# Kernel optimization log

Measured on AMD Instinct MI355X. Metric: run time of the kernel, lower is better.

## Reference

```python
import jax, jax.numpy as jnp
import numpy as np

NUM_CAPSULES = 10
NUM_ROUTES = 512
IN_CHANNELS = 8
OUT_CHANNELS = 16
BATCH = 512  # must equal NUM_ROUTES for the module's broadcast to be valid


def squash(x):
    # norm over last dim; v = ||s||^2/(1+||s||^2) * s/||s||
    norm = jnp.linalg.norm(x, axis=-1, keepdims=True)
    norm_sq = norm ** 2
    return norm_sq / (1.0 + norm_sq) * (x / norm)


def setup_inputs() -> dict:
    key = jax.random.key(0)
    k1, k2 = jax.random.split(key)
    x = jax.random.normal(k1, (BATCH, NUM_ROUTES, IN_CHANNELS), dtype=jnp.float32)
    route_weights = jax.random.normal(
        k2, (NUM_CAPSULES, NUM_ROUTES, IN_CHANNELS, OUT_CHANNELS), dtype=jnp.float32
    )
    return {"x": x, "route_weights": route_weights}


def reference(x, route_weights):
    B, R, Cin = x.shape
    # x -> [B, 1, R, Cin] (after view/unsqueeze/permute in the torch code)
    xb = x[:, None, :, :]
    # route_weights.permute(1,0,2,3) -> [R, num_caps, Cin, Cout]
    w = jnp.transpose(route_weights, (1, 0, 2, 3))
    # torch/jnp matmul broadcast of batch dims (B,1) vs (R,num_caps); B==R here.
    # u_hat[b, j] = x[b] @ w[route=b, cap=j]  -> [B, num_caps, R, Cout]
    u_hat = jnp.matmul(xb, w)
    b_ij = jnp.zeros(u_hat.shape[:3] + (1,), dtype=u_hat.dtype)
    for _ in range(3):  # fixed 3 routing iterations
        c_ij = jax.nn.softmax(b_ij, axis=2)            # softmax over routes
        s_j = jnp.sum(c_ij * u_hat, axis=2, keepdims=True)  # [B,J,1,Cout]
        v_j = squash(s_j)
        b_ij = b_ij + jnp.sum(u_hat * v_j, axis=-1, keepdims=True)
    return jnp.squeeze(v_j, axis=2)  # [B, num_caps, Cout]
```

## Files before the change

### kernel.cpp

```cpp
#include <hip/hip_runtime.h>
#include <math.h>

constexpr int BATCH = 512;
constexpr int NC    = 10;
constexpr int RR    = 512;
constexpr int CI    = 8;
constexpr int CO    = 16;

constexpr int TPB = 128;
constexpr int RPT = RR / TPB;

__global__ __launch_bounds__(TPB) void caps_route_kernel(
    const float* __restrict__ x,
    const float* __restrict__ rw,
    float* __restrict__ out)
{
    const int blk  = blockIdx.x;
    const int b    = blk / NC;
    const int c    = blk - b * NC;
    const int t    = threadIdx.x;
    const int lane = t & 63;
    const int wave = t >> 6;

    __shared__ __align__(16) float W[CI][CO];
    __shared__ __align__(16) float red[2][CO];
    __shared__ float sred[2];

    if (t < CI * CO) {
        ((float*)W)[t] = rw[((size_t)c * RR + b) * (CI * CO) + t];
    }
    __syncthreads();

    float xs[RPT][CI];
    #pragma unroll
    for (int k = 0; k < RPT; ++k) {
        const float4* xp = (const float4*)(x + ((size_t)b * RR + t + k * TPB) * CI);
        float4 a0 = xp[0], a1 = xp[1];
        xs[k][0]=a0.x; xs[k][1]=a0.y; xs[k][2]=a0.z; xs[k][3]=a0.w;
        xs[k][4]=a1.x; xs[k][5]=a1.y; xs[k][6]=a1.z; xs[k][7]=a1.w;
    }

    float u[RPT][CO];
    #pragma unroll
    for (int k = 0; k < RPT; ++k)
        #pragma unroll
        for (int o = 0; o < CO; ++o) u[k][o] = 0.f;

    #pragma unroll
    for (int i = 0; i < CI; ++i) {
        const float4* Wrow = (const float4*)&W[i][0];
        float4 wa = Wrow[0], wb = Wrow[1], wc = Wrow[2], wd = Wrow[3];
        #pragma unroll
        for (int k = 0; k < RPT; ++k) {
            const float xv = xs[k][i];
            u[k][0]  = fmaf(xv, wa.x, u[k][0]);
            u[k][1]  = fmaf(xv, wa.y, u[k][1]);
            u[k][2]  = fmaf(xv, wa.z, u[k][2]);
            u[k][3]  = fmaf(xv, wa.w, u[k][3]);
            u[k][4]  = fmaf(xv, wb.x, u[k][4]);
            u[k][5]  = fmaf(xv, wb.y, u[k][5]);
            u[k][6]  = fmaf(xv, wb.z, u[k][6]);
            u[k][7]  = fmaf(xv, wb.w, u[k][7]);
            u[k][8]  = fmaf(xv, wc.x, u[k][8]);
            u[k][9]  = fmaf(xv, wc.y, u[k][9]);
            u[k][10] = fmaf(xv, wc.z, u[k][10]);
            u[k][11] = fmaf(xv, wc.w, u[k][11]);
            u[k][12] = fmaf(xv, wd.x, u[k][12]);
            u[k][13] = fmaf(xv, wd.y, u[k][13]);
            u[k][14] = fmaf(xv, wd.z, u[k][14]);
            u[k][15] = fmaf(xv, wd.w, u[k][15]);
        }
    }

    float logit[RPT];
    #pragma unroll
    for (int k = 0; k < RPT; ++k) logit[k] = 0.f;

    float num[CO];
    float ks = 0.f;

    for (int iter = 0; iter < 3; ++iter) {
        float p[CO];
        float den_local = 0.f;
        if (iter == 0) {
            #pragma unroll
            for (int o = 0; o < CO; ++o)
                p[o] = (u[0][o] + u[1][o]) + (u[2][o] + u[3][o]);
        } else {
            float e[RPT];
            #pragma unroll
            for (int k = 0; k < RPT; ++k) e[k] = __expf(logit[k]);
            den_local = (e[0] + e[1]) + (e[2] + e[3]);
            #pragma unroll
            for (int o = 0; o < CO; ++o) {
                float a = fmaf(e[0], u[0][o], e[1] * u[1][o]);
                float d = fmaf(e[2], u[2][o], e[3] * u[3][o]);
                p[o] = a + d;
            }
        }

        float q1[8];
        {
            const bool hi = (lane & 32) != 0;
            #pragma unroll
            for (int k = 0; k < 8; ++k) {
                float keep = hi ? p[8 + k] : p[k];
                float send = hi ? p[k]     : p[8 + k];
                q1[k] = keep + __shfl_xor(send, 32, 64);
            }
        }
        float q2[4];
        {
            const bool hi = (lane & 16) != 0;
            #pragma unroll
            for (int k = 0; k < 4; ++k) {
                float keep = hi ? q1[4 + k] : q1[k];
                float send = hi ? q1[k]     : q1[4 + k];
                q2[k] = keep + __shfl_xor(send, 16, 64);
            }
        }
        float q3[2];
        {
            const bool hi = (lane & 8) != 0;
            #pragma unroll
            for (int k = 0; k < 2; ++k) {
                float keep = hi ? q2[2 + k] : q2[k];
                float send = hi ? q2[k]     : q2[2 + k];
                q3[k] = keep + __shfl_xor(send, 8, 64);
            }
        }
        float q4;
        {
            const bool hi = (lane & 4) != 0;
            float keep = hi ? q3[1] : q3[0];
            float send = hi ? q3[0] : q3[1];
            q4 = keep + __shfl_xor(send, 4, 64);
        }
        q4 += __shfl_xor(q4, 2, 64);
        q4 += __shfl_xor(q4, 1, 64);

        if (iter != 0) {
            den_local += __shfl_xor(den_local, 32, 64);
            den_local += __shfl_xor(den_local, 16, 64);
            den_local += __shfl_xor(den_local,  8, 64);
            den_local += __shfl_xor(den_local,  4, 64);
            den_local += __shfl_xor(den_local,  2, 64);
            den_local += __shfl_xor(den_local,  1, 64);
        }

        __syncthreads();
        if ((lane & 3) == 0) red[wave][lane >> 2] = q4;
        if (lane == 0)       sred[wave] = den_local;
        __syncthreads();

        {
            const float4* r0 = (const float4*)&red[0][0];
            const float4* r1 = (const float4*)&red[1][0];
            #pragma unroll
            for (int j = 0; j < 4; ++j) {
                float4 a = r0[j], d = r1[j];
                num[4*j+0] = a.x + d.x;
                num[4*j+1] = a.y + d.y;
                num[4*j+2] = a.z + d.z;
                num[4*j+3] = a.w + d.w;
            }
        }
        const float den = (iter == 0) ? (float)RR : (sred[0] + sred[1]);
        const float inv = 1.0f / den;

        #pragma unroll
        for (int o = 0; o < CO; ++o) num[o] *= inv;

        float nsq = 0.f;
        #pragma unroll
        for (int o = 0; o < CO; ++o) nsq = fmaf(num[o], num[o], nsq);
        const float nrm = sqrtf(nsq);
        ks = nrm / (1.0f + nsq);

        if (iter < 2) {
            #pragma unroll
            for (int k = 0; k < RPT; ++k) {
                float d = 0.f;
                #pragma unroll
                for (int o = 0; o < CO; ++o) d = fmaf(u[k][o], num[o], d);
                logit[k] = fmaf(d, ks, logit[k]);
            }
        }
    }

    if (t == 0) {
        float4* op = (float4*)(out + ((size_t)b * NC + c) * CO);
        op[0] = make_float4(num[0]*ks,  num[1]*ks,  num[2]*ks,  num[3]*ks);
        op[1] = make_float4(num[4]*ks,  num[5]*ks,  num[6]*ks,  num[7]*ks);
        op[2] = make_float4(num[8]*ks,  num[9]*ks,  num[10]*ks, num[11]*ks);
        op[3] = make_float4(num[12]*ks, num[13]*ks, num[14]*ks, num[15]*ks);
    }
}

extern "C" void kernel_launch(void* const* d_in, const int* in_sizes, int n_in,
                              void* d_out, int out_size, void* d_ws, size_t ws_size,
                              hipStream_t stream) {
    const float* x  = (const float*)d_in[0];
    const float* rw = (const float*)d_in[1];
    float* out = (float*)d_out;

    dim3 grid(BATCH * NC);
    dim3 block(TPB);
    caps_route_kernel<<<grid, block, 0, stream>>>(x, rw, out);
}
```

Measured before the change: 29.59 us.

## Use single-wave blocks with 8 routes per thread and shuffle-only reductions

Halves the block size to one 64-lane wave, so each thread now handles 8 routes instead of 4. The cross-wave LDS reduction and its two __syncthreads per routing iteration go away. The 16 reduced sums are broadcast with __shfl from the lanes that hold them, and the output store is spread over 4 lanes. The trade-off is half as many waves in flight and a larger per-thread register footprint (8x16 u values), which could reduce latency hiding or cause spills.

```diff
diff --git a/kernel.cpp b/kernel.cpp
--- a/kernel.cpp
+++ b/kernel.cpp
@@ -7,10 +7,10 @@
 constexpr int CI    = 8;
 constexpr int CO    = 16;
 
-constexpr int TPB = 128;
+constexpr int TPB = 64;
 constexpr int RPT = RR / TPB;
 
-__global__ __launch_bounds__(TPB) void caps_route_kernel(
+__global__ __launch_bounds__(TPB, 2) void caps_route_kernel(
     const float* __restrict__ x,
     const float* __restrict__ rw,
     float* __restrict__ out)
@@ -19,15 +19,13 @@
     const int b    = blk / NC;
     const int c    = blk - b * NC;
     const int t    = threadIdx.x;
-    const int lane = t & 63;
-    const int wave = t >> 6;
 
     __shared__ __align__(16) float W[CI][CO];
-    __shared__ __align__(16) float red[2][CO];
-    __shared__ float sred[2];
 
-    if (t < CI * CO) {
-        ((float*)W)[t] = rw[((size_t)c * RR + b) * (CI * CO) + t];
+    {
+        const size_t base = ((size_t)c * RR + b) * (CI * CO);
+        ((float*)W)[t]      = rw[base + t];
+        ((float*)W)[t + 64] = rw[base + t + 64];
     }
     __syncthreads();
 
@@ -81,27 +79,32 @@
 
     for (int iter = 0; iter < 3; ++iter) {
         float p[CO];
-        float den_local = 0.f;
+        float den = 0.f;
         if (iter == 0) {
             #pragma unroll
-            for (int o = 0; o < CO; ++o)
-                p[o] = (u[0][o] + u[1][o]) + (u[2][o] + u[3][o]);
+            for (int o = 0; o < CO; ++o) {
+                float a = (u[0][o] + u[1][o]) + (u[2][o] + u[3][o]);
+                float d = (u[4][o] + u[5][o]) + (u[6][o] + u[7][o]);
+                p[o] = a + d;
+            }
         } else {
             float e[RPT];
             #pragma unroll
             for (int k = 0; k < RPT; ++k) e[k] = __expf(logit[k]);
-            den_local = (e[0] + e[1]) + (e[2] + e[3]);
+            den = ((e[0] + e[1]) + (e[2] + e[3])) + ((e[4] + e[5]) + (e[6] + e[7]));
             #pragma unroll
             for (int o = 0; o < CO; ++o) {
                 float a = fmaf(e[0], u[0][o], e[1] * u[1][o]);
                 float d = fmaf(e[2], u[2][o], e[3] * u[3][o]);
-                p[o] = a + d;
+                float f = fmaf(e[4], u[4][o], e[5] * u[5][o]);
+                float g = fmaf(e[6], u[6][o], e[7] * u[7][o]);
+                p[o] = (a + d) + (f + g);
             }
         }
 
         float q1[8];
         {
-            const bool hi = (lane & 32) != 0;
+            const bool hi = (t & 32) != 0;
             #pragma unroll
             for (int k = 0; k < 8; ++k) {
                 float keep = hi ? p[8 + k] : p[k];
@@ -111,7 +114,7 @@
         }
         float q2[4];
         {
-            const bool hi = (lane & 16) != 0;
+            const bool hi = (t & 16) != 0;
             #pragma unroll
             for (int k = 0; k < 4; ++k) {
                 float keep = hi ? q1[4 + k] : q1[k];
@@ -121,7 +124,7 @@
         }
         float q3[2];
         {
-            const bool hi = (lane & 8) != 0;
+            const bool hi = (t & 8) != 0;
             #pragma unroll
             for (int k = 0; k < 2; ++k) {
                 float keep = hi ? q2[2 + k] : q2[k];
@@ -131,7 +134,7 @@
         }
         float q4;
         {
-            const bool hi = (lane & 4) != 0;
+            const bool hi = (t & 4) != 0;
             float keep = hi ? q3[1] : q3[0];
             float send = hi ? q3[0] : q3[1];
             q4 = keep + __shfl_xor(send, 4, 64);
@@ -140,32 +143,20 @@
         q4 += __shfl_xor(q4, 1, 64);
 
         if (iter != 0) {
-            den_local += __shfl_xor(den_local, 32, 64);
-            den_local += __shfl_xor(den_local, 16, 64);
-            den_local += __shfl_xor(den_local,  8, 64);
-            den_local += __shfl_xor(den_local,  4, 64);
-            den_local += __shfl_xor(den_local,  2, 64);
-            den_local += __shfl_xor(den_local,  1, 64);
+            den += __shfl_xor(den, 32, 64);
+            den += __shfl_xor(den, 16, 64);
+            den += __shfl_xor(den,  8, 64);
+            den += __shfl_xor(den,  4, 64);
+            den += __shfl_xor(den,  2, 64);
+            den += __shfl_xor(den,  1, 64);
+        } else {
+            den = (float)RR;
         }
 
-        __syncthreads();
-        if ((lane & 3) == 0) red[wave][lane >> 2] = q4;
-        if (lane == 0)       sred[wave] = den_local;
-        __syncthreads();
+        #pragma unroll
+        for (int o = 0; o < CO; ++o)
+            num[o] = __shfl(q4, o << 2, 64);
 
-        {
-            const float4* r0 = (const float4*)&red[0][0];
-            const float4* r1 = (const float4*)&red[1][0];
-            #pragma unroll
-            for (int j = 0; j < 4; ++j) {
-                float4 a = r0[j], d = r1[j];
-                num[4*j+0] = a.x + d.x;
-                num[4*j+1] = a.y + d.y;
-                num[4*j+2] = a.z + d.z;
-                num[4*j+3] = a.w + d.w;
-            }
-        }
-        const float den = (iter == 0) ? (float)RR : (sred[0] + sred[1]);
         const float inv = 1.0f / den;
 
         #pragma unroll
@@ -188,12 +179,10 @@
         }
     }
 
-    if (t == 0) {
+    if (t < 4) {
         float4* op = (float4*)(out + ((size_t)b * NC + c) * CO);
-        op[0] = make_float4(num[0]*ks,  num[1]*ks,  num[2]*ks,  num[3]*ks);
-        op[1] = make_float4(num[4]*ks,  num[5]*ks,  num[6]*ks,  num[7]*ks);
-        op[2] = make_float4(num[8]*ks,  num[9]*ks,  num[10]*ks, num[11]*ks);
-        op[3] = make_float4(num[12]*ks, num[13]*ks, num[14]*ks, num[15]*ks);
+        op[t] = make_float4(num[4*t+0]*ks, num[4*t+1]*ks,
+                            num[4*t+2]*ks, num[4*t+3]*ks);
     }
 }
 
```

Result: slower. 83.44 us (+182.0%).
